# Performance work log

Measured on AMD Instinct MI355X. Metric: run time of the kernel, lower is better.

The kernel has to match this reference:

```python
import jax, jax.numpy as jnp
import numpy as np

CH = 256
B, H, W = 8, 128, 128
CQK = CH // 8


def _conv1x1(x, w, b):
    # x: [B,C,H,W], w: [O,C], b: [O]
    return jnp.einsum('bchw,oc->bohw', x, w) + b[None, :, None, None]


def setup_inputs() -> dict:
    key = jax.random.key(0)
    ks = jax.random.split(key, 8)
    sq = 1.0 / np.sqrt(CH)
    return {
        'x': jax.random.normal(ks[0], (B, CH, H, W), dtype=jnp.float32),
        'Wq': jax.random.normal(ks[1], (CQK, CH), dtype=jnp.float32) * sq,
        'bq': jax.random.normal(ks[2], (CQK,), dtype=jnp.float32) * 0.01,
        'Wk': jax.random.normal(ks[3], (CQK, CH), dtype=jnp.float32) * sq,
        'bk': jax.random.normal(ks[4], (CQK,), dtype=jnp.float32) * 0.01,
        'Wv': jax.random.normal(ks[5], (CH, CH), dtype=jnp.float32) * sq,
        'bv': jax.random.normal(ks[6], (CH,), dtype=jnp.float32) * 0.01,
        'gamma': jax.random.normal(ks[7], (1,), dtype=jnp.float32) * 0.1,
        'recurrence': 2,
    }


def reference(x, Wq, bq, Wk, bk, Wv, bv, gamma, recurrence):
    q = _conv1x1(x, Wq, bq)   # [B, C//8, H, W]
    k = _conv1x1(x, Wk, bk)   # [B, C//8, H, W]
    v = _conv1x1(x, Wv, bv)   # [B, C, H, W]
    if recurrence % 2 == 1:
        # attention along W, independently per (b, h); no mask
        energy = jnp.einsum('bchi,bchj->bhij', q, k)      # [B,H,W,W]
        att = jax.nn.softmax(energy, axis=-1)
        out = jnp.einsum('bchj,bhij->bchi', v, att)       # [B,C,H,W]
    else:
        # attention along H, independently per (b, w); diagonal masked -inf
        energy = jnp.einsum('bciw,bcjw->bwij', q, k)      # [B,W,H,H]
        h = energy.shape[-1]
        diag = jnp.eye(h, dtype=bool)[None, None]
        energy = jnp.where(diag, -jnp.inf, energy)
        att = jax.nn.softmax(energy, axis=-1)             # [B,W,H,H]
        out = jnp.einsum('bcjw,bwij->bciw', v, att)       # [B,C,H,W]
    return gamma[0] * out + x
```

## Files before the change

kernel.cpp:

```cpp
#include <hip/hip_runtime.h>
#include <hip/hip_bf16.h>

#define B_   8
#define CH_  256
#define CQK_ 32
#define H_   128
#define W_   128

typedef __attribute__((ext_vector_type(8))) short s16x8;
typedef __attribute__((ext_vector_type(4))) float f32x4;
typedef __attribute__((ext_vector_type(4))) unsigned short u16x4;

__device__ __forceinline__ unsigned short f2b(float f) {
  __hip_bfloat16 h = __float2bfloat16(f);
  return *(unsigned short*)&h;
}
__device__ __forceinline__ float b2f(unsigned short u) {
  return __uint_as_float(((unsigned)u) << 16);
}


__global__ void kw_pack(const float* __restrict__ Wq, const float* __restrict__ Wk,
                        const float* __restrict__ Wv, unsigned short* __restrict__ wqk,
                        unsigned short* __restrict__ wv) {
  int idx = blockIdx.x * 256 + threadIdx.x;
  if (idx < 64 * 256) {
    int qc = idx >> 8, c = idx & 255;
    wqk[idx] = f2b(qc < 32 ? Wq[qc * 256 + c] : Wk[(qc - 32) * 256 + c]);
  } else {
    int i2 = idx - 64 * 256;
    wv[i2] = f2b(Wv[i2]);
  }
}

__global__ __launch_bounds__(256) void k0_xpose(const float* __restrict__ x,
                                                unsigned short* __restrict__ xt) {
  __shared__ unsigned short st[256 * 137];
  const int t = threadIdx.x;
  const int b = blockIdx.x >> 7;
  const int h = blockIdx.x & 127;
  const float* xin = x + ((size_t)b * 256 * 128 + h) * 128;
  const int w = t & 127, chalf = t >> 7;
#pragma unroll 8
  for (int it = 0; it < 128; ++it) {
    int c = it * 2 + chalf;
    st[c * 137 + w] = f2b(xin[(size_t)c * 16384 + w]);
  }
  __syncthreads();
  unsigned short* xo = xt + ((size_t)b * 128 * 128 + h) * 256;
  const int cl = t & 127, whalf = t >> 7;
#pragma unroll 8
  for (int it = 0; it < 64; ++it) {
    int wr = it * 2 + whalf;
    unsigned v = (unsigned)st[(2 * cl) * 137 + wr] |
                 ((unsigned)st[(2 * cl + 1) * 137 + wr] << 16);
    *(unsigned*)&xo[(size_t)wr * 32768 + 2 * cl] = v;
  }
}

__global__ __launch_bounds__(256, 2) void k0b_xpose(const unsigned short* __restrict__ xt,
                                                    unsigned short* __restrict__ xt2) {
  __shared__ unsigned short st[128 * 264];
  const int t = threadIdx.x;
  const size_t colbase = (size_t)blockIdx.x * 32768;
#pragma unroll
  for (int it = 0; it < 16; ++it) {
    int ch = it * 256 + t;
    int row = ch >> 5, off = (ch & 31) * 8;
    *(uint4*)&st[row * 264 + off] = *(const uint4*)&xt[colbase + ch * 8];
  }
  __syncthreads();
  const int hpl = t & 3, cq = t >> 2;
#pragma unroll 8
  for (int it = 0; it < 64; ++it) {
    const int itc = it & 3, ith = it >> 2;
    const int c = itc * 64 + cq;
    const int hp = ith * 4 + hpl;
    unsigned v = (unsigned)st[(2 * hp) * 264 + c] |
                 ((unsigned)st[(2 * hp + 1) * 264 + c] << 16);
    *(unsigned*)&xt2[colbase + (size_t)c * 128 + hp * 2] = v;
  }
}

__device__ __forceinline__ void gld_lds16(const unsigned short* g, unsigned short* l) {
  __builtin_amdgcn_global_load_lds(
      (const __attribute__((address_space(1))) void*)g,
      (__attribute__((address_space(3))) void*)l, 16, 0, 0);
}

__device__ __forceinline__ void stage_tile(const unsigned short* __restrict__ gsrc,
                                           unsigned short* lds, int k0,
                                           int wv_id, int lane) {
#pragma unroll
  for (int i = 0; i < 4; ++i) {
    const int chunk = wv_id * 4 + i;
    const int L = chunk * 1024 + lane * 16;
    const int row = L >> 7;
    const int sb = L & 127;
    const int srcb = sb ^ ((row & 7) << 4);
    gld_lds16(gsrc + row * 256 + k0 + (srcb >> 1), lds + chunk * 512);
  }
}

struct SmemY {
  unsigned short qt[128 * 40];
  unsigned short kt[128 * 40];
  union {
    unsigned short att[128 * 136];
    unsigned short xstage[2][128 * 64];
  } u;
};

__global__ __launch_bounds__(256, 2)
void k1y(const unsigned short* __restrict__ xt, const unsigned short* __restrict__ xt2,
         const unsigned short* __restrict__ wqk, const float* __restrict__ bq,
         const float* __restrict__ bk, unsigned short* __restrict__ y) {
  __shared__ SmemY sm;
  const int t = threadIdx.x;
  const int wvid = t >> 6;
  const int lane = t & 63;
  const int l15 = lane & 15;
  const int quad = lane >> 4;
  const int b = blockIdx.x >> 7;
  const int w = blockIdx.x & 127;
  const size_t colbase = ((size_t)b * 128 + w) * 32768;

  {
    const int qc0 = wvid * 16;
    f32x4 acc[8];
#pragma unroll
    for (int nt = 0; nt < 8; ++nt) acc[nt] = {0.f, 0.f, 0.f, 0.f};
    const unsigned short* arow = wqk + (qc0 + l15) * 256 + quad * 8;
    const unsigned short* gcol = xt + colbase;
    stage_tile(gcol, sm.u.xstage[0], 0, wvid, lane);
    __syncthreads();
#pragma unroll
    for (int kc = 0; kc < 4; ++kc) {
      const int cur = kc & 1;
      if (kc < 3) stage_tile(gcol, sm.u.xstage[cur ^ 1], (kc + 1) * 64, wvid, lane);
#pragma unroll
      for (int kk2 = 0; kk2 < 2; ++kk2) {
        s16x8 a = *(const s16x8*)(arow + (kc * 2 + kk2) * 32);
#pragma unroll
        for (int nt = 0; nt < 8; ++nt) {
          const int row = nt * 16 + l15;
          const int col = (kk2 * 64 + quad * 16) ^ ((row & 7) << 4);
          s16x8 bb = *(const s16x8*)((const char*)sm.u.xstage[cur] + row * 128 + col);
          acc[nt] = __builtin_amdgcn_mfma_f32_16x16x32_bf16(a, bb, acc[nt], 0, 0, 0);
        }
      }
      __syncthreads();
    }
    const float* bp = (wvid < 2) ? bq : bk;
    const int qcl = qc0 & 16;
    float bias[4];
#pragma unroll
    for (int r = 0; r < 4; ++r) bias[r] = bp[qcl + quad * 4 + r];
    unsigned short* dst = (wvid < 2) ? sm.qt : sm.kt;
#pragma unroll
    for (int nt = 0; nt < 8; ++nt) {
      int h = nt * 16 + l15;
      u16x4 pk;
#pragma unroll
      for (int r = 0; r < 4; ++r) pk[r] = f2b(acc[nt][r] + bias[r]);
      *(u16x4*)&dst[h * 40 + qcl + quad * 4] = pk;
    }
  }
  __syncthreads();

  {
    const int i0 = wvid * 32;
    s16x8 aQ[2];
#pragma unroll
    for (int mt = 0; mt < 2; ++mt)
      aQ[mt] = *(const s16x8*)&sm.qt[(i0 + mt * 16 + l15) * 40 + quad * 8];
    f32x4 eacc[2][8];
#pragma unroll
    for (int mt = 0; mt < 2; ++mt)
#pragma unroll
      for (int nt = 0; nt < 8; ++nt) eacc[mt][nt] = {0.f, 0.f, 0.f, 0.f};
#pragma unroll
    for (int nt = 0; nt < 8; ++nt) {
      s16x8 bK = *(const s16x8*)&sm.kt[(nt * 16 + l15) * 40 + quad * 8];
      eacc[0][nt] = __builtin_amdgcn_mfma_f32_16x16x32_bf16(aQ[0], bK, eacc[0][nt], 0, 0, 0);
      eacc[1][nt] = __builtin_amdgcn_mfma_f32_16x16x32_bf16(aQ[1], bK, eacc[1][nt], 0, 0, 0);
    }
#pragma unroll
    for (int mt = 0; mt < 2; ++mt)
#pragma unroll
      for (int nt = 0; nt < 8; ++nt) {
        const int j = nt * 16 + l15;
#pragma unroll
        for (int r = 0; r < 4; ++r)
          if (j == i0 + mt * 16 + quad * 4 + r) eacc[mt][nt][r] = -__builtin_inff();
      }
#pragma unroll
    for (int mt = 0; mt < 2; ++mt)
#pragma unroll
      for (int r = 0; r < 4; ++r) {
        float mx = -__builtin_inff();
#pragma unroll
        for (int nt = 0; nt < 8; ++nt) mx = fmaxf(mx, eacc[mt][nt][r]);
        mx = fmaxf(mx, __shfl_xor(mx, 1));
        mx = fmaxf(mx, __shfl_xor(mx, 2));
        mx = fmaxf(mx, __shfl_xor(mx, 4));
        mx = fmaxf(mx, __shfl_xor(mx, 8));
        float s = 0.f;
#pragma unroll
        for (int nt = 0; nt < 8; ++nt) {
          float p = __expf(eacc[mt][nt][r] - mx);
          eacc[mt][nt][r] = p;
          s += p;
        }
        s += __shfl_xor(s, 1);
        s += __shfl_xor(s, 2);
        s += __shfl_xor(s, 4);
        s += __shfl_xor(s, 8);
        const float inv = 1.0f / s;
        const int i = i0 + mt * 16 + quad * 4 + r;
#pragma unroll
        for (int nt = 0; nt < 8; ++nt)
          sm.u.att[i * 136 + nt * 16 + l15] = f2b(eacc[mt][nt][r] * inv);
      }
  }
  __syncthreads();

  f32x4 yacc[8][4];
#pragma unroll
  for (int mt = 0; mt < 8; ++mt)
#pragma unroll
    for (int nt = 0; nt < 4; ++nt) yacc[mt][nt] = {0.f, 0.f, 0.f, 0.f};
  {
    const int c0 = wvid * 64;
#pragma unroll
    for (int kj = 0; kj < 4; ++kj) {
      s16x8 aP[8];
#pragma unroll
      for (int mt = 0; mt < 8; ++mt)
        aP[mt] = *(const s16x8*)&sm.u.att[(mt * 16 + l15) * 136 + kj * 32 + quad * 8];
#pragma unroll
      for (int nt = 0; nt < 4; ++nt) {
        s16x8 bX = *(const s16x8*)&xt2[colbase + (size_t)(c0 + nt * 16 + l15) * 128 +
                                        kj * 32 + quad * 8];
#pragma unroll
        for (int mt = 0; mt < 8; ++mt)
          yacc[mt][nt] = __builtin_amdgcn_mfma_f32_16x16x32_bf16(aP[mt], bX, yacc[mt][nt], 0, 0, 0);
      }
    }
  }
#pragma unroll 1
  for (int h2 = 0; h2 < 2; ++h2) {
    __syncthreads();
    if ((wvid >> 1) == h2) {
      const int clb = (wvid & 1) * 64;
#pragma unroll
      for (int mt = 0; mt < 8; ++mt)
#pragma unroll
        for (int nt = 0; nt < 4; ++nt) {
          const int cl = clb + nt * 16 + l15;
#pragma unroll
          for (int r = 0; r < 4; ++r)
            sm.u.att[(mt * 16 + quad * 4 + r) * 136 + cl] = f2b(yacc[mt][nt][r]);
        }
    }
    __syncthreads();
#pragma unroll
    for (int it = 0; it < 8; ++it) {
      int g = it * 256 + t;
      int i = g >> 4, cc = (g & 15) * 8;
      *(uint4*)&y[((size_t)(b * 128 + i) * 128 + w) * 256 + h2 * 128 + cc] =
          *(const uint4*)&sm.u.att[i * 136 + cc];
    }
  }
}


struct SmemG {
  unsigned short A[2][128 * 64];
  unsigned short B[2][128 * 64];
};

__global__ __launch_bounds__(256, 2)
void k2g(const unsigned short* __restrict__ y, const unsigned short* __restrict__ wv,
         const float* __restrict__ bv, const float* __restrict__ gamma,
         const float* __restrict__ x, float* __restrict__ out) {
  __shared__ SmemG sm;
  const int t = threadIdx.x;
  const int wv_id = t >> 6;
  const int lane = t & 63;
  const int l15 = lane & 15;
  const int quad = lane >> 4;
  const int mhalf = (blockIdx.x >> 3) & 1;
  const int bh = ((blockIdx.x >> 4) << 3) | (blockIdx.x & 7);
  const int b = bh >> 7, h = bh & 127;
  const unsigned short* gA = wv + mhalf * 128 * 256;
  const unsigned short* gB = y + (size_t)bh * 128 * 256;
  const int wr = wv_id >> 1;
  const int wc = wv_id & 1;

  f32x4 acc[4][4];
#pragma unroll
  for (int mt = 0; mt < 4; ++mt)
#pragma unroll
    for (int nt = 0; nt < 4; ++nt) acc[mt][nt] = {0.f, 0.f, 0.f, 0.f};
  float xpf[4][4][4];

  stage_tile(gA, sm.A[0], 0, wv_id, lane);
  stage_tile(gB, sm.B[0], 0, wv_id, lane);
  __syncthreads();

#pragma unroll
  for (int kt = 0; kt < 4; ++kt) {
    const int cur = kt & 1;
    if (kt < 3) {
      stage_tile(gA, sm.A[cur ^ 1], (kt + 1) * 64, wv_id, lane);
      stage_tile(gB, sm.B[cur ^ 1], (kt + 1) * 64, wv_id, lane);
    }
    {
      const int mt = kt;
#pragma unroll
      for (int r = 0; r < 4; ++r) {
        const int co = mhalf * 128 + wr * 64 + mt * 16 + quad * 4 + r;
        const float* xp = x + ((size_t)(b * 256 + co) * 128 + h) * 128 + wc * 64 + l15;
#pragma unroll
        for (int nt = 0; nt < 4; ++nt) xpf[mt][r][nt] = xp[nt * 16];
      }
    }
#pragma unroll
    for (int ks = 0; ks < 2; ++ks) {
      s16x8 a[4], bb[4];
#pragma unroll
      for (int mt = 0; mt < 4; ++mt) {
        const int row = wr * 64 + mt * 16 + l15;
        const int col = (ks * 64 + quad * 16) ^ ((row & 7) << 4);
        a[mt] = *(const s16x8*)((const char*)&sm.A[cur][0] + row * 128 + col);
      }
#pragma unroll
      for (int nt = 0; nt < 4; ++nt) {
        const int row = wc * 64 + nt * 16 + l15;
        const int col = (ks * 64 + quad * 16) ^ ((row & 7) << 4);
        bb[nt] = *(const s16x8*)((const char*)&sm.B[cur][0] + row * 128 + col);
      }
#pragma unroll
      for (int nt = 0; nt < 4; ++nt)
#pragma unroll
        for (int mt = 0; mt < 4; ++mt)
          acc[mt][nt] = __builtin_amdgcn_mfma_f32_16x16x32_bf16(a[mt], bb[nt], acc[mt][nt], 0, 0, 0);
    }
    __syncthreads();
  }

  const float g = gamma[0];
#pragma unroll
  for (int mt = 0; mt < 4; ++mt)
#pragma unroll
    for (int r = 0; r < 4; ++r) {
      const int co = mhalf * 128 + wr * 64 + mt * 16 + quad * 4 + r;
      const float bvv = bv[co];
      const size_t base = ((size_t)(b * 256 + co) * 128 + h) * 128;
#pragma unroll
      for (int nt = 0; nt < 4; ++nt) {
        const int wcol = wc * 64 + nt * 16 + l15;
        out[base + wcol] = g * (acc[mt][nt][r] + bvv) + xpf[mt][r][nt];
      }
    }
}


struct SmemK1 {
  __hip_bfloat16 x[CH_][H_];
  float att[H_][130];
  union {
    struct { __hip_bfloat16 q[CQK_][H_]; __hip_bfloat16 k[CQK_][H_]; } qk;
    float vchunk[32][130];
  } s;
};

__device__ __forceinline__ void load_bf16x16(const __hip_bfloat16* p, float* f) {
  const uint4* p4 = (const uint4*)p;
  uint4 a = p4[0], b = p4[1];
  unsigned uu[8] = {a.x, a.y, a.z, a.w, b.x, b.y, b.z, b.w};
#pragma unroll
  for (int m = 0; m < 8; ++m) {
    f[2 * m] = __uint_as_float(uu[m] << 16);
    f[2 * m + 1] = __uint_as_float(uu[m] & 0xffff0000u);
  }
}

__global__ __launch_bounds__(256, 1)
void k1_attn(const float* __restrict__ x, const float* __restrict__ Wq,
             const float* __restrict__ bq, const float* __restrict__ Wk,
             const float* __restrict__ bk, const float* __restrict__ Wv,
             const float* __restrict__ bv, float* __restrict__ o_t) {
  __shared__ SmemK1 sm;
  const int t = threadIdx.x;
  const int b = blockIdx.x >> 7;
  const int w = blockIdx.x & 127;
  {
    const float* xb = x + (size_t)b * CH_ * H_ * W_ + w;
    const int h = t & 127;
    const int c0 = (t >> 7) * 128;
#pragma unroll 8
    for (int r = 0; r < 128; ++r) {
      const int c = c0 + r;
      sm.x[c][h] = __float2bfloat16(xb[(size_t)(c * H_ + h) * W_]);
    }
  }
  __syncthreads();
  {
    const int qc = t >> 3;
    const int i0 = (t & 7) << 4;
    float qa[16], ka[16];
    const float bqv = bq[qc], bkv = bk[qc];
#pragma unroll
    for (int u = 0; u < 16; ++u) { qa[u] = bqv; ka[u] = bkv; }
    const float* wqr = Wq + qc * CH_;
    const float* wkr = Wk + qc * CH_;
    for (int c = 0; c < CH_; c += 4) {
      const float4 wq4 = *(const float4*)(wqr + c);
      const float4 wk4 = *(const float4*)(wkr + c);
      const float wqs[4] = {wq4.x, wq4.y, wq4.z, wq4.w};
      const float wks[4] = {wk4.x, wk4.y, wk4.z, wk4.w};
#pragma unroll
      for (int cc = 0; cc < 4; ++cc) {
        float xf[16];
        load_bf16x16(&sm.x[c + cc][i0], xf);
#pragma unroll
        for (int u = 0; u < 16; ++u) {
          qa[u] += wqs[cc] * xf[u];
          ka[u] += wks[cc] * xf[u];
        }
      }
    }
#pragma unroll
    for (int u = 0; u < 16; ++u) {
      sm.s.qk.q[qc][i0 + u] = __float2bfloat16(qa[u]);
      sm.s.qk.k[qc][i0 + u] = __float2bfloat16(ka[u]);
    }
  }
  __syncthreads();
  {
    const int i = t >> 1;
    const int j0 = (t & 1) << 6;
    float qreg[32];
#pragma unroll
    for (int qc = 0; qc < 32; ++qc) qreg[qc] = __bfloat162float(sm.s.qk.q[qc][i]);
    float e[64];
#pragma unroll
    for (int u = 0; u < 64; ++u) e[u] = 0.0f;
    for (int qc = 0; qc < 32; ++qc) {
#pragma unroll
      for (int jc = 0; jc < 4; ++jc) {
        float kf[16];
        load_bf16x16(&sm.s.qk.k[qc][j0 + jc * 16], kf);
#pragma unroll
        for (int u = 0; u < 16; ++u) e[jc * 16 + u] += qreg[qc] * kf[u];
      }
    }
    if (i >= j0 && i < j0 + 64) e[i - j0] = -__builtin_inff();
    float m = -__builtin_inff();
#pragma unroll
    for (int u = 0; u < 64; ++u) m = fmaxf(m, e[u]);
    m = fmaxf(m, __shfl_xor(m, 1));
    float ssum = 0.0f;
#pragma unroll
    for (int u = 0; u < 64; ++u) { e[u] = __expf(e[u] - m); ssum += e[u]; }
    ssum += __shfl_xor(ssum, 1);
    const float inv = 1.0f / ssum;
#pragma unroll
    for (int u = 0; u < 64; u += 2)
      *(float2*)&sm.att[i][j0 + u] = make_float2(e[u] * inv, e[u + 1] * inv);
  }
  __syncthreads();
  const int vcc = t >> 3;
  const int vj0 = (t & 7) << 4;
  const int ai0 = (t >> 3) << 2;
  const int acc0 = (t & 7) << 2;
  for (int ch = 0; ch < 8; ++ch) {
    {
      const int cg = ch * 32 + vcc;
      float acc[16];
      const float bvv = bv[cg];
#pragma unroll
      for (int u = 0; u < 16; ++u) acc[u] = bvv;
      const float* wvr = Wv + (size_t)cg * CH_;
      for (int c = 0; c < CH_; c += 4) {
        const float4 w4 = *(const float4*)(wvr + c);
        const float ws4[4] = {w4.x, w4.y, w4.z, w4.w};
#pragma unroll
        for (int cc = 0; cc < 4; ++cc) {
          float xf[16];
          load_bf16x16(&sm.x[c + cc][vj0], xf);
#pragma unroll
          for (int u = 0; u < 16; ++u) acc[u] += ws4[cc] * xf[u];
        }
      }
#pragma unroll
      for (int m2 = 0; m2 < 8; ++m2)
        *(float2*)&sm.s.vchunk[vcc][vj0 + 2 * m2] = make_float2(acc[2 * m2], acc[2 * m2 + 1]);
    }
    __syncthreads();
    {
      float oacc[4][4];
#pragma unroll
      for (int s2 = 0; s2 < 4; ++s2)
#pragma unroll
        for (int u = 0; u < 4; ++u) oacc[s2][u] = 0.0f;
#pragma unroll 4
      for (int j = 0; j < H_; j += 2) {
        float2 av[4], vv[4];
#pragma unroll
        for (int u = 0; u < 4; ++u) av[u] = *(const float2*)&sm.att[ai0 + u][j];
#pragma unroll
        for (int s2 = 0; s2 < 4; ++s2) vv[s2] = *(const float2*)&sm.s.vchunk[acc0 + s2][j];
#pragma unroll
        for (int s2 = 0; s2 < 4; ++s2)
#pragma unroll
          for (int u = 0; u < 4; ++u)
            oacc[s2][u] += vv[s2].x * av[u].x + vv[s2].y * av[u].y;
      }
#pragma unroll
      for (int s2 = 0; s2 < 4; ++s2) {
        const int cg = ch * 32 + acc0 + s2;
        float4 st;
        st.x = oacc[s2][0]; st.y = oacc[s2][1]; st.z = oacc[s2][2]; st.w = oacc[s2][3];
        *(float4*)&o_t[(((size_t)b * CH_ + cg) * W_ + w) * H_ + ai0] = st;
      }
    }
    __syncthreads();
  }
}

__global__ __launch_bounds__(256)
void k2_epi(const float* __restrict__ o_t, const float* __restrict__ x,
            const float* __restrict__ gamma, float* __restrict__ out) {
  const int pr = blockIdx.x % 10;
  const int plane = blockIdx.x / 10;
  const int rT[10] = {0, 0, 0, 0, 1, 1, 1, 2, 2, 3};
  const int sT[10] = {0, 1, 2, 3, 1, 2, 3, 2, 3, 3};
  const int r = rT[pr], s = sT[pr];
  __shared__ float t1[32][33];
  __shared__ float t2[32][33];
  const int t = threadIdx.x;
  const size_t pbase = (size_t)plane * (H_ * W_);
  const float* ob = o_t + pbase;
#pragma unroll
  for (int ii = 0; ii < 4; ++ii) {
    const int idx = ii * 256 + t;
    const int ww = idx >> 5, hh = idx & 31;
    t1[ww][hh] = ob[(s * 32 + ww) * H_ + (r * 32 + hh)];
    if (r != s) t2[ww][hh] = ob[(r * 32 + ww) * H_ + (s * 32 + hh)];
  }
  __syncthreads();
  const float g = gamma[0];
#pragma unroll
  for (int ii = 0; ii < 4; ++ii) {
    const int idx = ii * 256 + t;
    const int hh = idx >> 5, ww = idx & 31;
    const size_t o1 = pbase + (size_t)(r * 32 + hh) * W_ + (s * 32 + ww);
    out[o1] = g * t1[ww][hh] + x[o1];
    if (r != s) {
      const size_t o2 = pbase + (size_t)(s * 32 + hh) * W_ + (r * 32 + ww);
      out[o2] = g * t2[ww][hh] + x[o2];
    }
  }
}


extern "C" void kernel_launch(void* const* d_in, const int* in_sizes, int n_in,
                              void* d_out, int out_size, void* d_ws, size_t ws_size,
                              hipStream_t stream) {
  const float* x     = (const float*)d_in[0];
  const float* Wq    = (const float*)d_in[1];
  const float* bq    = (const float*)d_in[2];
  const float* Wk    = (const float*)d_in[3];
  const float* bk    = (const float*)d_in[4];
  const float* Wv    = (const float*)d_in[5];
  const float* bv    = (const float*)d_in[6];
  const float* gamma = (const float*)d_in[7];
  float* out = (float*)d_out;

  const size_t XT   = (size_t)B_ * W_ * H_ * CH_ * 2;
  const size_t YT   = XT;
  const size_t WQKB = 64 * 256 * 2;
  const size_t WVB  = 256 * 256 * 2;
  const size_t FAST_WS = XT + YT + WQKB + WVB;

  if (ws_size >= FAST_WS) {
    unsigned short* xt  = (unsigned short*)d_ws;
    unsigned short* yb  = (unsigned short*)((char*)d_ws + XT);
    unsigned short* wqk = (unsigned short*)((char*)d_ws + XT + YT);
    unsigned short* wvb = (unsigned short*)((char*)d_ws + XT + YT + WQKB);
    unsigned short* xt2 = (unsigned short*)d_out;
    hipLaunchKernelGGL(kw_pack, dim3(320), dim3(256), 0, stream, Wq, Wk, Wv, wqk, wvb);
    hipLaunchKernelGGL(k0_xpose, dim3(B_ * H_), dim3(256), 0, stream, x, xt);
    hipLaunchKernelGGL(k0b_xpose, dim3(B_ * W_), dim3(256), 0, stream, xt, xt2);
    hipLaunchKernelGGL(k1y, dim3(B_ * W_), dim3(256), 0, stream,
                       xt, xt2, wqk, bq, bk, yb);
    hipLaunchKernelGGL(k2g, dim3(B_ * H_ * 2), dim3(256), 0, stream,
                       yb, wvb, bv, gamma, x, out);
  } else {
    const size_t OT_F = (size_t)B_ * CH_ * H_ * W_ * sizeof(float);
    float* o_t = (ws_size >= OT_F) ? (float*)d_ws : out;
    hipLaunchKernelGGL(k1_attn, dim3(B_ * W_), dim3(256), 0, stream,
                       x, Wq, bq, Wk, bk, Wv, bv, o_t);
    hipLaunchKernelGGL(k2_epi, dim3((B_ * CH_) * 10), dim3(256), 0, stream,
                       o_t, x, gamma, out);
  }
}
```

Measured before the change: 373.5 us.

## Halve k2g K-tile to raise occupancy and defer residual x loads to epilogue

The second GEMM kernel now stages 32-wide K tiles instead of 64-wide, with a new swizzle. This halves LDS use per block and allows launch bounds of 4 blocks per SM. The residual x prefetch into 64 registers during the main loop is removed, and x is instead read directly in the epilogue, cutting register pressure. The trade-off is twice as many K iterations and barriers, and x load latency is no longer hidden behind the MFMA loop.

Result: slower. 389.8 us (+4.4%).

```diff
diff --git a/kernel.cpp b/kernel.cpp
--- a/kernel.cpp
+++ b/kernel.cpp
@@ -98,6 +98,20 @@
     const int row = L >> 7;
     const int sb = L & 127;
     const int srcb = sb ^ ((row & 7) << 4);
+    gld_lds16(gsrc + row * 256 + k0 + (srcb >> 1), lds + chunk * 512);
+  }
+}
+
+__device__ __forceinline__ void stage_tile32(const unsigned short* __restrict__ gsrc,
+                                             unsigned short* lds, int k0,
+                                             int wv_id, int lane) {
+#pragma unroll
+  for (int i = 0; i < 2; ++i) {
+    const int chunk = wv_id * 2 + i;
+    const int L = chunk * 1024 + lane * 16;
+    const int row = L >> 6;
+    const int sb = L & 63;
+    const int srcb = sb ^ (((row >> 1) & 3) << 4);
     gld_lds16(gsrc + row * 256 + k0 + (srcb >> 1), lds + chunk * 512);
   }
 }
@@ -276,11 +290,11 @@
 
 
 struct SmemG {
-  unsigned short A[2][128 * 64];
-  unsigned short B[2][128 * 64];
+  unsigned short A[2][128 * 32];
+  unsigned short B[2][128 * 32];
 };
 
-__global__ __launch_bounds__(256, 2)
+__global__ __launch_bounds__(256, 4)
 void k2g(const unsigned short* __restrict__ y, const unsigned short* __restrict__ wv,
          const float* __restrict__ bv, const float* __restrict__ gamma,
          const float* __restrict__ x, float* __restrict__ out) {
@@ -303,43 +317,31 @@
   for (int mt = 0; mt < 4; ++mt)
 #pragma unroll
     for (int nt = 0; nt < 4; ++nt) acc[mt][nt] = {0.f, 0.f, 0.f, 0.f};
-  float xpf[4][4][4];
-
-  stage_tile(gA, sm.A[0], 0, wv_id, lane);
-  stage_tile(gB, sm.B[0], 0, wv_id, lane);
-  __syncthreads();
-
-#pragma unroll
-  for (int kt = 0; kt < 4; ++kt) {
+
+  stage_tile32(gA, sm.A[0], 0, wv_id, lane);
+  stage_tile32(gB, sm.B[0], 0, wv_id, lane);
+  __syncthreads();
+
+#pragma unroll
+  for (int kt = 0; kt < 8; ++kt) {
     const int cur = kt & 1;
-    if (kt < 3) {
-      stage_tile(gA, sm.A[cur ^ 1], (kt + 1) * 64, wv_id, lane);
-      stage_tile(gB, sm.B[cur ^ 1], (kt + 1) * 64, wv_id, lane);
+    if (kt < 7) {
+      stage_tile32(gA, sm.A[cur ^ 1], (kt + 1) * 32, wv_id, lane);
+      stage_tile32(gB, sm.B[cur ^ 1], (kt + 1) * 32, wv_id, lane);
     }
     {
-      const int mt = kt;
-#pragma unroll
-      for (int r = 0; r < 4; ++r) {
-        const int co = mhalf * 128 + wr * 64 + mt * 16 + quad * 4 + r;
-        const float* xp = x + ((size_t)(b * 256 + co) * 128 + h) * 128 + wc * 64 + l15;
-#pragma unroll
-        for (int nt = 0; nt < 4; ++nt) xpf[mt][r][nt] = xp[nt * 16];
-      }
-    }
-#pragma unroll
-    for (int ks = 0; ks < 2; ++ks) {
       s16x8 a[4], bb[4];
 #pragma unroll
       for (int mt = 0; mt < 4; ++mt) {
         const int row = wr * 64 + mt * 16 + l15;
-        const int col = (ks * 64 + quad * 16) ^ ((row & 7) << 4);
-        a[mt] = *(const s16x8*)((const char*)&sm.A[cur][0] + row * 128 + col);
+        const int col = (quad * 16) ^ (((row >> 1) & 3) << 4);
+        a[mt] = *(const s16x8*)((const char*)&sm.A[cur][0] + row * 64 + col);
       }
 #pragma unroll
       for (int nt = 0; nt < 4; ++nt) {
         const int row = wc * 64 + nt * 16 + l15;
-        const int col = (ks * 64 + quad * 16) ^ ((row & 7) << 4);
-        bb[nt] = *(const s16x8*)((const char*)&sm.B[cur][0] + row * 128 + col);
+        const int col = (quad * 16) ^ (((row >> 1) & 3) << 4);
+        bb[nt] = *(const s16x8*)((const char*)&sm.B[cur][0] + row * 64 + col);
       }
 #pragma unroll
       for (int nt = 0; nt < 4; ++nt)
@@ -347,7 +349,7 @@
         for (int mt = 0; mt < 4; ++mt)
           acc[mt][nt] = __builtin_amdgcn_mfma_f32_16x16x32_bf16(a[mt], bb[nt], acc[mt][nt], 0, 0, 0);
     }
-    __syncthreads();
+    if (kt < 7) __syncthreads();
   }
 
   const float g = gamma[0];
@@ -361,7 +363,7 @@
 #pragma unroll
       for (int nt = 0; nt < 4; ++nt) {
         const int wcol = wc * 64 + nt * 16 + l15;
-        out[base + wcol] = g * (acc[mt][nt][r] + bvv) + xpf[mt][r][nt];
+        out[base + wcol] = g * (acc[mt][nt][r] + bvv) + x[base + wcol];
       }
     }
 }
```
